# Kernel tuning notes

Hardware: AMD Instinct MI355X
Metric: run time of the kernel (lower is better)

Reference implementation:

```python
import jax, jax.numpy as jnp
import numpy as np

N_NODES = 50000
N_EDGES = 800000
FEAT = 128
OUT = 128
BATCH = 2


def setup_inputs() -> dict:
    key = jax.random.key(0)
    k_h, k_w1, k_w2, k_a, k_src, k_dst = jax.random.split(key, 6)
    h = jax.random.normal(k_h, (BATCH, N_NODES, FEAT), dtype=jnp.float32)
    # xavier-uniform-ish scale for params
    W1 = jax.random.normal(k_w1, (FEAT, FEAT), dtype=jnp.float32) * (1.414 / np.sqrt(FEAT))
    W2 = jax.random.normal(k_w2, (FEAT, OUT), dtype=jnp.float32) * (1.414 / np.sqrt(FEAT))
    a = jax.random.normal(k_a, (2 * FEAT, 1), dtype=jnp.float32) * 0.05
    src = jax.random.randint(k_src, (N_EDGES,), 0, N_NODES, dtype=jnp.int32)
    dst = jax.random.randint(k_dst, (N_EDGES,), 0, N_NODES, dtype=jnp.int32)
    return {"h": h, "W1": W1, "W2": W2, "a": a, "src": src, "dst": dst}


def reference(h, W1, W2, a, src, dst):
    B, N, F = h.shape
    g = jnp.einsum('bnf,fk->bnk', h, W1)                      # [B,N,F]
    # cat([g_i, g_j]) @ a  ==  g_i @ a[:F] + g_j @ a[F:]
    s_i = g @ a[:F, 0]                                        # [B,N]
    s_j = g @ a[F:, 0]                                        # [B,N]
    e = jax.nn.leaky_relu(s_i[:, src] + s_j[:, dst], 0.2)     # [B,E]
    # segment softmax over edges grouped by src node
    eT = e.T                                                  # [E,B]
    m = jax.ops.segment_max(eT, src, num_segments=N)          # [N,B]
    ex = jnp.exp(eT - m[src])                                 # [E,B]
    denom = jax.ops.segment_sum(ex, src, num_segments=N)      # [N,B]
    alpha = (ex / denom[src]).T                               # [B,E]
    msg = g[:, dst] * alpha[..., None]                        # [B,E,F]
    h_prime = jnp.zeros_like(g).at[:, src].add(msg)           # scatter-add onto src
    return jax.nn.relu(jnp.einsum('bnf,fo->bno', h_prime, W2))
```

## Files before the change

kernel.cpp:

```cpp
#include <hip/hip_runtime.h>
#include <hip/hip_bf16.h>
#include <hip/hip_fp16.h>
#include <cfloat>

#define N_NODES 50000
#define N_EDGES 800000
#define FEAT 128
#define BATCH 2
#define RTOT (BATCH*N_NODES)

typedef __bf16 bf16x8 __attribute__((ext_vector_type(8)));
typedef float  f32x4  __attribute__((ext_vector_type(4)));

__device__ inline unsigned short f2bf(float f){
  unsigned int u = __float_as_uint(f);
  u = (u + 0x7fffu + ((u >> 16) & 1u)) >> 16;
  return (unsigned short)u;
}

__global__ void k_prep(const float* __restrict__ W1, const float* __restrict__ W2,
                       __bf16* __restrict__ W1t, __bf16* __restrict__ W2t,
                       int* __restrict__ cnt){
  int i = blockIdx.x*blockDim.x + threadIdx.x;
  if(i < FEAT*FEAT){
    int k = i >> 7, col = i & 127;
    int sw = (col << 7) + (k ^ ((col & 7) << 3));
    W1t[sw] = (__bf16)W1[i];
    W2t[sw] = (__bf16)W2[i];
  }
  if(i < N_NODES) cnt[i] = 0;
}

__global__ __launch_bounds__(256) void k_gemm1_mfma(const float* __restrict__ h,
        const __bf16* __restrict__ W1t, const float* __restrict__ a,
        __bf16* __restrict__ g, float* __restrict__ s_i, float* __restrict__ s_j,
        const int* __restrict__ src, int* __restrict__ cnt)
{
  __shared__ __bf16 Bs[FEAT*FEAT];
  int t = threadIdx.x, lane = t & 63, wid = t >> 6;
  {
    const float4* srcp = (const float4*)W1t;
    float4* dstp = (float4*)Bs;
    for(int i = t; i < FEAT*FEAT/8; i += 256) dstp[i] = srcp[i];
  }
  __syncthreads();

  int rb = blockIdx.x*64 + wid*16;
  int r  = rb + (lane & 15);
  int kq = (lane >> 4) * 8;

  bf16x8 af[4];
  if(r < RTOT){
    const float* hrow = h + (size_t)r*FEAT + kq;
    #pragma unroll
    for(int ks = 0; ks < 4; ks++){
      float4 p0 = *(const float4*)(hrow + ks*32);
      float4 p1 = *(const float4*)(hrow + ks*32 + 4);
      bf16x8 v;
      v[0]=(__bf16)p0.x; v[1]=(__bf16)p0.y; v[2]=(__bf16)p0.z; v[3]=(__bf16)p0.w;
      v[4]=(__bf16)p1.x; v[5]=(__bf16)p1.y; v[6]=(__bf16)p1.z; v[7]=(__bf16)p1.w;
      af[ks] = v;
    }
  } else {
    #pragma unroll
    for(int ks = 0; ks < 4; ks++){ bf16x8 z = {}; af[ks] = z; }
  }

  f32x4 acc[8] = {};
  #pragma unroll
  for(int cb = 0; cb < 8; cb++){
    int col = cb*16 + (lane & 15);
    int swbase = (col << 7);
    int swx = ((col & 7) << 3);
    #pragma unroll
    for(int ks = 0; ks < 4; ks++){
      int kb = ks*32 + kq;
      bf16x8 bf = *(const bf16x8*)&Bs[swbase + (kb ^ swx)];
      acc[cb] = __builtin_amdgcn_mfma_f32_16x16x32_bf16(af[ks], bf, acc[cb], 0, 0, 0);
    }
  }

  int hgrp = lane >> 4;
  float pi[4] = {0,0,0,0}, pj[4] = {0,0,0,0};
  #pragma unroll
  for(int cb = 0; cb < 8; cb++){
    int col = cb*16 + (lane & 15);
    float al = a[col], ah = a[FEAT + col];
    #pragma unroll
    for(int reg = 0; reg < 4; reg++){
      int row = rb + hgrp*4 + reg;
      float v = acc[cb][reg];
      if(row < RTOT){
        int b = (row >= N_NODES) ? 1 : 0;
        int n = row - b*N_NODES;
        g[(size_t)n*256 + b*128 + col] = (__bf16)v;
      }
      pi[reg] = fmaf(v, al, pi[reg]);
      pj[reg] = fmaf(v, ah, pj[reg]);
    }
  }
  #pragma unroll
  for(int reg = 0; reg < 4; reg++){
    #pragma unroll
    for(int m = 1; m < 16; m <<= 1){
      pi[reg] += __shfl_xor(pi[reg], m, 64);
      pj[reg] += __shfl_xor(pj[reg], m, 64);
    }
  }
  if((lane & 15) == 0){
    #pragma unroll
    for(int reg = 0; reg < 4; reg++){
      int row = rb + hgrp*4 + reg;
      if(row < RTOT){
        int b = (row >= N_NODES) ? 1 : 0;
        int n = row - b*N_NODES;
        s_i[n*2 + b] = pi[reg];
        s_j[n*2 + b] = pj[reg];
      }
    }
  }

  int gs = gridDim.x * 256;
  for(int e = blockIdx.x*256 + t; e < N_EDGES; e += gs)
    atomicAdd(&cnt[src[e]], 1);
}

__global__ __launch_bounds__(1024) void k_scan1(const int* __restrict__ cnt,
                                                int* __restrict__ off, int* __restrict__ bsum){
  __shared__ int s[1024];
  int t = threadIdx.x, idx = blockIdx.x*1024 + t;
  int v = (idx < N_NODES) ? cnt[idx] : 0;
  s[t] = v; __syncthreads();
  for(int st = 1; st < 1024; st <<= 1){
    int u = (t >= st) ? s[t-st] : 0;
    __syncthreads();
    s[t] += u;
    __syncthreads();
  }
  if(idx < N_NODES) off[idx] = s[t] - v;
  if(t == 1023) bsum[blockIdx.x] = s[t];
}
__global__ __launch_bounds__(1024) void k_scan2(int* __restrict__ off,
                                                const int* __restrict__ bsum, int* __restrict__ curs){
  __shared__ int pfx;
  int t = threadIdx.x, idx = blockIdx.x*1024 + t;
  if(t < 64){
    int nb = (N_NODES + 1023)/1024;
    int v0 = (t < nb) ? bsum[t] : 0;
    int v = v0;
    for(int st = 1; st < 64; st <<= 1){
      int u = __shfl_up(v, st, 64);
      if(t >= st) v += u;
    }
    if(t == blockIdx.x) pfx = v - v0;
  }
  __syncthreads();
  if(idx < N_NODES){
    int o = off[idx] + pfx;
    off[idx] = o;
    curs[idx] = o;
  }
}
__global__ void k_fill(const int* __restrict__ src, const int* __restrict__ dst,
                       int* __restrict__ curs, int* __restrict__ dste){
  int e = blockIdx.x*blockDim.x + threadIdx.x;
  if(e < N_EDGES){ int pos = atomicAdd(&curs[src[e]], 1); dste[pos] = dst[e]; }
}

__global__ __launch_bounds__(512) void k_agg2(const unsigned int* __restrict__ g,
     const float* __restrict__ s_i, const float* __restrict__ s_j,
     const int* __restrict__ cnt, const int* __restrict__ off,
     const int* __restrict__ dste, const __bf16* __restrict__ W2t,
     float* __restrict__ out)
{
  __shared__ __bf16 Bs[FEAT*FEAT];
  __shared__ __bf16 hpT[16*FEAT];
  int t = threadIdx.x, lane = t & 63, w = t >> 6;
  {
    const float4* srcp = (const float4*)W2t;
    float4* dstp = (float4*)Bs;
    for(int i = t; i < FEAT*FEAT/8; i += 512) dstp[i] = srcp[i];
  }

  int n = blockIdx.x*8 + w;
  int deg = cnt[n], o0 = off[n];
  int half = lane >> 5, li = lane & 31;
  float si = s_i[n*2 + half];
  int selp = lane & 32;

  float denom = 0.f;
  float a0=0.f, a1=0.f, a2=0.f, a3=0.f;

  for(int base=0; base<deg; base+=32){
    int i = base + li;
    unsigned int wv = 0;
    if(i < deg){
      int d = dste[o0 + i];
      float xx = si + s_j[d*2 + half];
      float x = (xx > 0.f) ? xx : 0.2f*xx;
      float p = __expf(x);
      denom += p;
      wv = ((unsigned int)__half_as_ushort(__float2half(p)) << 16) | (unsigned int)d;
    }
    int lim = min(32, deg-base);
    int lim8 = (lim + 7) & ~7;
    for(int j=0; j<lim8; j+=8){
      unsigned int ww[8];
      #pragma unroll
      for(int c=0;c<8;c++) ww[c] = __shfl(wv, selp | (j+c), 64);
      uint2 u[8]; float q[8];
      #pragma unroll
      for(int c=0;c<8;c++){
        q[c] = __half2float(__ushort_as_half((unsigned short)(ww[c] >> 16)));
        u[c] = *(const uint2*)(g + (size_t)(ww[c] & 0xffffu)*128 + lane*2);
      }
      #pragma unroll
      for(int c=0;c<8;c++){
        a0 = fmaf(q[c], __uint_as_float(u[c].x << 16),         a0);
        a1 = fmaf(q[c], __uint_as_float(u[c].x & 0xffff0000u), a1);
        a2 = fmaf(q[c], __uint_as_float(u[c].y << 16),         a2);
        a3 = fmaf(q[c], __uint_as_float(u[c].y & 0xffff0000u), a3);
      }
    }
  }
  #pragma unroll
  for(int mm=16; mm; mm>>=1) denom += __shfl_xor(denom, mm, 64);
  float inv = (denom > 0.f) ? 1.0f/denom : 0.f;

  {
    int ri = w*2 + half;
    int gidx = li >> 1;
    int gsw = gidx ^ (ri & 7);
    int coff = gsw*8 + (li & 1)*4;
    unsigned int w0 = ((unsigned int)f2bf(a1*inv) << 16) | f2bf(a0*inv);
    unsigned int w1 = ((unsigned int)f2bf(a3*inv) << 16) | f2bf(a2*inv);
    uint2 o; o.x = w0; o.y = w1;
    *(uint2*)&hpT[ri*FEAT + coff] = o;
  }
  __syncthreads();

  int r  = lane & 15;
  int kq16 = lane >> 4;
  bf16x8 af[4];
  #pragma unroll
  for(int ks = 0; ks < 4; ks++){
    int gr = ks*4 + kq16;
    int gsw2 = gr ^ (r & 7);
    af[ks] = *(const bf16x8*)&hpT[r*FEAT + gsw2*8];
  }
  f32x4 acc = {};
  int col = w*16 + (lane & 15);
  int swbase = (col << 7);
  int swx = ((col & 7) << 3);
  #pragma unroll
  for(int ks = 0; ks < 4; ks++){
    int kb = ks*32 + kq16*8;
    bf16x8 bf = *(const bf16x8*)&Bs[swbase + (kb ^ swx)];
    acc = __builtin_amdgcn_mfma_f32_16x16x32_bf16(af[ks], bf, acc, 0, 0, 0);
  }
  int hgrp = lane >> 4;
  #pragma unroll
  for(int reg = 0; reg < 4; reg++){
    int rri = hgrp*4 + reg;
    int node = blockIdx.x*8 + (rri >> 1);
    int b = rri & 1;
    out[(size_t)(b*N_NODES + node)*FEAT + col] = fmaxf(acc[reg], 0.f);
  }
}

extern "C" void kernel_launch(void* const* d_in, const int* in_sizes, int n_in,
                              void* d_out, int out_size, void* d_ws, size_t ws_size,
                              hipStream_t stream) {
  const float* h  = (const float*)d_in[0];
  const float* W1 = (const float*)d_in[1];
  const float* W2 = (const float*)d_in[2];
  const float* a  = (const float*)d_in[3];
  const int* src  = (const int*)d_in[4];
  const int* dst  = (const int*)d_in[5];
  float* out = (float*)d_out;

  char* w = (char*)d_ws;
  __bf16* g   = (__bf16*)w;                          w += (size_t)RTOT*FEAT*2;
  float* s_i  = (float*)w;                           w += (size_t)RTOT*4;
  float* s_j  = (float*)w;                           w += (size_t)RTOT*4;
  __bf16* W1t = (__bf16*)w;                          w += FEAT*FEAT*2;
  __bf16* W2t = (__bf16*)w;                          w += FEAT*FEAT*2;
  int* cnt  = (int*)w;                               w += N_NODES*4;
  int* off  = (int*)w;                               w += N_NODES*4;
  int* curs = (int*)w;                               w += N_NODES*4;
  int* dste = (int*)w;                               w += N_EDGES*4;
  int* bsum = (int*)w;

  k_prep<<<(N_NODES+255)/256,256,0,stream>>>(W1,W2,W1t,W2t,cnt);

  int gemm_grid = (RTOT + 63)/64;
  k_gemm1_mfma<<<gemm_grid,256,0,stream>>>(h,W1t,a,g,s_i,s_j,src,cnt);

  int nb = (N_NODES+1023)/1024;
  k_scan1<<<nb,1024,0,stream>>>(cnt,off,bsum);
  k_scan2<<<nb,1024,0,stream>>>(off,bsum,curs);
  k_fill<<<(N_EDGES+255)/256,256,0,stream>>>(src,dst,curs,dste);

  k_agg2<<<N_NODES/8,512,0,stream>>>((const unsigned int*)g,s_i,s_j,cnt,off,dste,W2t,out);
}
```

Measured before the change: 166.4 us.

## Transpose MFMA outputs for vectorized stores and merge scan kernels

Swaps the MFMA operand order in both GEMM kernels so each lane holds four consecutive columns of one row. This allows packed 8-byte bf16 stores of g, float4 output stores, and a two-step shuffle reduction for the attention scores instead of scattered scalar stores. The two-pass scan becomes one kernel in which each block recomputes its prefix by summing earlier counts, which removes one launch. The aggregation kernel now reads degree from off[n+1]-off[n], and off gains a sentinel entry. The price is redundant prefix work that grows with the block index.

```diff
diff --git a/kernel.cpp b/kernel.cpp
--- a/kernel.cpp
+++ b/kernel.cpp
@@ -47,7 +47,8 @@
 
   int rb = blockIdx.x*64 + wid*16;
   int r  = rb + (lane & 15);
-  int kq = (lane >> 4) * 8;
+  int hgrp = lane >> 4;
+  int kq = hgrp * 8;
 
   bf16x8 af[4];
   if(r < RTOT){
@@ -76,48 +77,32 @@
     for(int ks = 0; ks < 4; ks++){
       int kb = ks*32 + kq;
       bf16x8 bf = *(const bf16x8*)&Bs[swbase + (kb ^ swx)];
-      acc[cb] = __builtin_amdgcn_mfma_f32_16x16x32_bf16(af[ks], bf, acc[cb], 0, 0, 0);
-    }
-  }
-
-  int hgrp = lane >> 4;
-  float pi[4] = {0,0,0,0}, pj[4] = {0,0,0,0};
-  #pragma unroll
-  for(int cb = 0; cb < 8; cb++){
-    int col = cb*16 + (lane & 15);
-    float al = a[col], ah = a[FEAT + col];
-    #pragma unroll
-    for(int reg = 0; reg < 4; reg++){
-      int row = rb + hgrp*4 + reg;
-      float v = acc[cb][reg];
-      if(row < RTOT){
-        int b = (row >= N_NODES) ? 1 : 0;
-        int n = row - b*N_NODES;
-        g[(size_t)n*256 + b*128 + col] = (__bf16)v;
-      }
-      pi[reg] = fmaf(v, al, pi[reg]);
-      pj[reg] = fmaf(v, ah, pj[reg]);
-    }
-  }
-  #pragma unroll
-  for(int reg = 0; reg < 4; reg++){
-    #pragma unroll
-    for(int m = 1; m < 16; m <<= 1){
-      pi[reg] += __shfl_xor(pi[reg], m, 64);
-      pj[reg] += __shfl_xor(pj[reg], m, 64);
-    }
-  }
-  if((lane & 15) == 0){
-    #pragma unroll
-    for(int reg = 0; reg < 4; reg++){
-      int row = rb + hgrp*4 + reg;
-      if(row < RTOT){
-        int b = (row >= N_NODES) ? 1 : 0;
-        int n = row - b*N_NODES;
-        s_i[n*2 + b] = pi[reg];
-        s_j[n*2 + b] = pj[reg];
-      }
-    }
+      acc[cb] = __builtin_amdgcn_mfma_f32_16x16x32_bf16(bf, af[ks], acc[cb], 0, 0, 0);
+    }
+  }
+
+  if(r < RTOT){
+    int b = (r >= N_NODES) ? 1 : 0;
+    int n = r - b*N_NODES;
+    __bf16* grow = g + (size_t)n*256 + b*128;
+    float pi = 0.f, pj = 0.f;
+    #pragma unroll
+    for(int cb = 0; cb < 8; cb++){
+      int c0 = cb*16 + hgrp*4;
+      float4 al = *(const float4*)&a[c0];
+      float4 ah = *(const float4*)&a[FEAT + c0];
+      pi = fmaf(acc[cb][0], al.x, pi); pj = fmaf(acc[cb][0], ah.x, pj);
+      pi = fmaf(acc[cb][1], al.y, pi); pj = fmaf(acc[cb][1], ah.y, pj);
+      pi = fmaf(acc[cb][2], al.z, pi); pj = fmaf(acc[cb][2], ah.z, pj);
+      pi = fmaf(acc[cb][3], al.w, pi); pj = fmaf(acc[cb][3], ah.w, pj);
+      uint2 w;
+      w.x = ((unsigned int)f2bf(acc[cb][1]) << 16) | f2bf(acc[cb][0]);
+      w.y = ((unsigned int)f2bf(acc[cb][3]) << 16) | f2bf(acc[cb][2]);
+      *(uint2*)(grow + c0) = w;
+    }
+    pi += __shfl_xor(pi, 16, 64); pj += __shfl_xor(pj, 16, 64);
+    pi += __shfl_xor(pi, 32, 64); pj += __shfl_xor(pj, 32, 64);
+    if(hgrp == 0){ s_i[n*2 + b] = pi; s_j[n*2 + b] = pj; }
   }
 
   int gs = gridDim.x * 256;
@@ -125,10 +110,26 @@
     atomicAdd(&cnt[src[e]], 1);
 }
 
-__global__ __launch_bounds__(1024) void k_scan1(const int* __restrict__ cnt,
-                                                int* __restrict__ off, int* __restrict__ bsum){
+__global__ __launch_bounds__(1024) void k_scan(const int* __restrict__ cnt,
+                                               int* __restrict__ off, int* __restrict__ curs){
   __shared__ int s[1024];
-  int t = threadIdx.x, idx = blockIdx.x*1024 + t;
+  __shared__ int wsum[16];
+  __shared__ int pfx;
+  int t = threadIdx.x, b = blockIdx.x;
+  int ps = 0;
+  int lim = b*1024;
+  for(int i = t; i < lim; i += 1024) ps += cnt[i];
+  #pragma unroll
+  for(int mm=32; mm; mm>>=1) ps += __shfl_xor(ps, mm, 64);
+  if((t & 63) == 0) wsum[t >> 6] = ps;
+  __syncthreads();
+  if(t == 0){
+    int P = 0;
+    #pragma unroll
+    for(int w = 0; w < 16; w++) P += wsum[w];
+    pfx = P;
+  }
+  int idx = b*1024 + t;
   int v = (idx < N_NODES) ? cnt[idx] : 0;
   s[t] = v; __syncthreads();
   for(int st = 1; st < 1024; st <<= 1){
@@ -137,30 +138,14 @@
     s[t] += u;
     __syncthreads();
   }
-  if(idx < N_NODES) off[idx] = s[t] - v;
-  if(t == 1023) bsum[blockIdx.x] = s[t];
-}
-__global__ __launch_bounds__(1024) void k_scan2(int* __restrict__ off,
-                                                const int* __restrict__ bsum, int* __restrict__ curs){
-  __shared__ int pfx;
-  int t = threadIdx.x, idx = blockIdx.x*1024 + t;
-  if(t < 64){
-    int nb = (N_NODES + 1023)/1024;
-    int v0 = (t < nb) ? bsum[t] : 0;
-    int v = v0;
-    for(int st = 1; st < 64; st <<= 1){
-      int u = __shfl_up(v, st, 64);
-      if(t >= st) v += u;
-    }
-    if(t == blockIdx.x) pfx = v - v0;
-  }
-  __syncthreads();
   if(idx < N_NODES){
-    int o = off[idx] + pfx;
+    int o = pfx + s[t] - v;
     off[idx] = o;
     curs[idx] = o;
   }
-}
+  if(b == 0 && t == 0) off[N_NODES] = N_EDGES;
+}
+
 __global__ void k_fill(const int* __restrict__ src, const int* __restrict__ dst,
                        int* __restrict__ curs, int* __restrict__ dste){
   int e = blockIdx.x*blockDim.x + threadIdx.x;
@@ -169,7 +154,7 @@
 
 __global__ __launch_bounds__(512) void k_agg2(const unsigned int* __restrict__ g,
      const float* __restrict__ s_i, const float* __restrict__ s_j,
-     const int* __restrict__ cnt, const int* __restrict__ off,
+     const int* __restrict__ off,
      const int* __restrict__ dste, const __bf16* __restrict__ W2t,
      float* __restrict__ out)
 {
@@ -183,7 +168,7 @@
   }
 
   int n = blockIdx.x*8 + w;
-  int deg = cnt[n], o0 = off[n];
+  int o0 = off[n], deg = off[n+1] - o0;
   int half = lane >> 5, li = lane & 31;
   float si = s_i[n*2 + half];
   int selp = lane & 32;
@@ -256,15 +241,15 @@
   for(int ks = 0; ks < 4; ks++){
     int kb = ks*32 + kq16*8;
     bf16x8 bf = *(const bf16x8*)&Bs[swbase + (kb ^ swx)];
-    acc = __builtin_amdgcn_mfma_f32_16x16x32_bf16(af[ks], bf, acc, 0, 0, 0);
-  }
-  int hgrp = lane >> 4;
-  #pragma unroll
-  for(int reg = 0; reg < 4; reg++){
-    int rri = hgrp*4 + reg;
-    int node = blockIdx.x*8 + (rri >> 1);
-    int b = rri & 1;
-    out[(size_t)(b*N_NODES + node)*FEAT + col] = fmaxf(acc[reg], 0.f);
+    acc = __builtin_amdgcn_mfma_f32_16x16x32_bf16(bf, af[ks], acc, 0, 0, 0);
+  }
+  {
+    int node = blockIdx.x*8 + (r >> 1);
+    int b = r & 1;
+    float4 o;
+    o.x = fmaxf(acc[0], 0.f); o.y = fmaxf(acc[1], 0.f);
+    o.z = fmaxf(acc[2], 0.f); o.w = fmaxf(acc[3], 0.f);
+    *(float4*)&out[(size_t)(b*N_NODES + node)*FEAT + w*16 + kq16*4] = o;
   }
 }
 
@@ -286,10 +271,9 @@
   __bf16* W1t = (__bf16*)w;                          w += FEAT*FEAT*2;
   __bf16* W2t = (__bf16*)w;                          w += FEAT*FEAT*2;
   int* cnt  = (int*)w;                               w += N_NODES*4;
-  int* off  = (int*)w;                               w += N_NODES*4;
+  int* off  = (int*)w;                               w += (N_NODES+1)*4;
   int* curs = (int*)w;                               w += N_NODES*4;
   int* dste = (int*)w;                               w += N_EDGES*4;
-  int* bsum = (int*)w;
 
   k_prep<<<(N_NODES+255)/256,256,0,stream>>>(W1,W2,W1t,W2t,cnt);
 
@@ -297,9 +281,8 @@
   k_gemm1_mfma<<<gemm_grid,256,0,stream>>>(h,W1t,a,g,s_i,s_j,src,cnt);
 
   int nb = (N_NODES+1023)/1024;
-  k_scan1<<<nb,1024,0,stream>>>(cnt,off,bsum);
-  k_scan2<<<nb,1024,0,stream>>>(off,bsum,curs);
+  k_scan<<<nb,1024,0,stream>>>(cnt,off,curs);
   k_fill<<<(N_EDGES+255)/256,256,0,stream>>>(src,dst,curs,dste);
 
-  k_agg2<<<N_NODES/8,512,0,stream>>>((const unsigned int*)g,s_i,s_j,cnt,off,dste,W2t,out);
-}
+  k_agg2<<<N_NODES/8,512,0,stream>>>((const unsigned int*)g,s_i,s_j,off,dste,W2t,out);
+}
```

Result: slower. 172.6 us (+3.7%).
